# Kernel optimization log

Measured on AMD Instinct MI355X. Metric: run time of the kernel, lower is better.

Reference implementation:

```python
import jax, jax.numpy as jnp
import numpy as np

N = 65536          # query points (rays * samples per chunk)
C = 2048           # num_codes in code cloud
K = 16             # knn neighbors
CD = 64            # code_dim
IN_XYZ = 63        # positional-encoded xyz channels
IN_DIR = 27        # positional-encoded dir channels
W = 128            # decoder width (D=4, skips=[2])
DIST_SCALE = 2.0


def setup_inputs() -> dict:
    key = jax.random.key(0)
    ks = jax.random.split(key, 16)

    def glorot(k, shape):
        return jax.random.normal(k, shape, jnp.float32) / np.float32(np.sqrt(shape[0]))

    in_x = CD + IN_XYZ  # decoder in_channels_xyz = 127
    inp = {
        "indices": jnp.zeros((1,), jnp.int32),
        "query_points": jax.random.uniform(ks[0], (N, 3), jnp.float32),
        "xyzdir_embedded": jax.random.normal(ks[1], (N, IN_XYZ + IN_DIR), jnp.float32),
        "codes_position": jax.random.uniform(ks[2], (1, C, 3), jnp.float32),
        "codes": jax.random.normal(ks[3], (1, C, CD), jnp.float32) * 0.01,
        # decoder params
        "W0": glorot(ks[4], (in_x, W)), "b0": jnp.zeros((W,), jnp.float32),
        "W1": glorot(ks[5], (W, W)), "b1": jnp.zeros((W,), jnp.float32),
        "W2": glorot(ks[6], (W + in_x, W)), "b2": jnp.zeros((W,), jnp.float32),  # skip layer i=2
        "W3": glorot(ks[7], (W, W)), "b3": jnp.zeros((W,), jnp.float32),
        "Wf": glorot(ks[8], (W, W)), "bf": jnp.zeros((W,), jnp.float32),          # xyz_encoding_final
        "Wd": glorot(ks[9], (W + IN_DIR, W // 2)), "bd": jnp.zeros((W // 2,), jnp.float32),
        "Ws": glorot(ks[10], (W, 1)), "bs": jnp.zeros((1,), jnp.float32),
        "Wr": glorot(ks[11], (W // 2, 3)), "br": jnp.zeros((3,), jnp.float32),
    }
    return inp


def _knn_idx(q, c, k):
    # brute-force L2 knn (faiss replacement); indices only, no grad (torch no_grad)
    q = jax.lax.stop_gradient(q)
    c = jax.lax.stop_gradient(c)
    d2 = (jnp.sum(q * q, -1, keepdims=True)
          - 2.0 * q @ c.T
          + jnp.sum(c * c, -1))  # (N, C)
    _, idx = jax.lax.top_k(-d2, k)  # (N, K) nearest
    return idx


def reference(indices, query_points, xyzdir_embedded, codes_position, codes,
              W0, b0, W1, b1, W2, b2, W3, b3, Wf, bf, Wd, bd, Ws, bs, Wr, br):
    # --- CodeCloud.query ---
    cp = codes_position[indices][0]      # (C, 3)
    cc = codes[indices][0]               # (C, CD)
    idx = _knn_idx(query_points, cp, K)  # (N, K)
    neigh_pos = cp[idx]                  # (N, K, 3)
    sq = jnp.sum((query_points[:, None, :] - neigh_pos) ** 2, -1) + 1e-16  # (N, K)
    w = 1.0 / jnp.sqrt(sq) ** DIST_SCALE
    w = w / jnp.sum(w, -1, keepdims=True)
    neigh_codes = cc[idx]                # (N, K, CD)
    query_codes = jnp.einsum("nk,nkd->nd", w, neigh_codes)  # (N, CD)

    # --- IM_Decoder (D=4, W=128, skips=[2]) ---
    x = jnp.concatenate([query_codes, xyzdir_embedded], -1)  # (N, 127+27)
    in_x = CD + IN_XYZ
    input_xyz, input_dir = x[:, :in_x], x[:, in_x:]
    h = jax.nn.relu(input_xyz @ W0 + b0)
    h = jax.nn.relu(h @ W1 + b1)
    h = jax.nn.relu(jnp.concatenate([input_xyz, h], -1) @ W2 + b2)  # skip at i=2
    h = jax.nn.relu(h @ W3 + b3)
    sigma = h @ Ws + bs                       # (N, 1)
    final = h @ Wf + bf                       # (N, W)
    d = jax.nn.relu(jnp.concatenate([final, input_dir], -1) @ Wd + bd)
    rgb = d @ Wr + br                         # (N, 3)
    return jnp.concatenate([rgb, sigma], -1)  # (N, 4)
```

## Files before the change

### kernel.cpp

```cpp
#include <hip/hip_runtime.h>

#define N_Q   65536
#define N_C   2048
#define KNN_K 16
#define CDIM  64
#define SLCAP 128
#define KINF  0x7FFFFFFF

typedef _Float16 half_t;
typedef float v4f __attribute__((ext_vector_type(4)));
typedef half_t v8h __attribute__((ext_vector_type(8)));

#define ASTRIDE 136
#define DSTRIDE 40

__global__ void wtrans_kernel(const float* W0, const float* W1, const float* W2,
                              const float* W3, const float* Wf, const float* Wd,
                              const int* indices, const float* cpos,
                              half_t* wt, float4* cpos4){
  int idx = blockIdx.x * 256 + threadIdx.x;
  if (idx >= 110592) return;
  if (idx >= 108544){
    int i = idx - 108544;
    const float* cp = cpos + (size_t)indices[0] * N_C * 3;
    float x = cp[i*3 + 0], y = cp[i*3 + 1], z = cp[i*3 + 2];
    cpos4[i] = make_float4(x, y, z, fmaf(x, x, fmaf(y, y, fmaf(z, z, 4.0f))));
    return;
  }
  int base, nt, mode;
  const float* src = W1;
  if (idx < 16384){ base = 0; nt = 8; mode = 1; }
  else if (idx < 32768){ base = 16384; nt = 8; mode = 0; src = W1; }
  else if (idx < 65536){ base = 32768; nt = 8; mode = 2; }
  else if (idx < 81920){ base = 65536; nt = 8; mode = 0; src = W3; }
  else if (idx < 98304){ base = 81920; nt = 8; mode = 0; src = Wf; }
  else { base = 98304; nt = 4; mode = 3; }
  int i = idx - base;
  int tile = i >> 9, e = i & 511;
  int lane = e >> 3, j = e & 7;
  int k0idx = tile / nt, tcol = tile - k0idx*nt;
  int n = tcol*16 + (lane & 15);
  int k = k0idx*32 + ((lane >> 4) << 3) + j;
  float val;
  if (mode == 0)      val = src[k*128 + n];
  else if (mode == 1) val = (k < 127) ? W0[k*128 + n] : 0.f;
  else if (mode == 2) val = (k == 127) ? 0.f
                           : ((k < 127) ? W2[k*128 + n] : W2[(k-1)*128 + n]);
  else                val = (k < 155) ? Wd[k*64 + n] : 0.f;
  wt[idx] = (half_t)val;
}

__global__ __launch_bounds__(512, 8) void knn_kernel(const int* indices,
    const float* qpts, const float4* cpos4, const float* codes,
    const float* xyzdir, half_t* Ain, half_t* Din){
  __shared__ float4 lp[N_C];
  __shared__ int    sl[8*SLCAP];
  int tid = threadIdx.x;
  int lane = tid & 63, wave = tid >> 6;
  int l = lane & 15;
  const float* cc = codes + (size_t)indices[0] * N_C * CDIM;

  for (int c = tid; c < N_C; c += 512) lp[c] = cpos4[c];
  __syncthreads();

  int q = blockIdx.x * 8 + wave;
  float qx = qpts[q*3 + 0];
  float qy = qpts[q*3 + 1];
  float qz = qpts[q*3 + 2];
  float nqx = -2.0f*qx, nqy = -2.0f*qy, nqz = -2.0f*qz;

  int p[32];
#pragma unroll
  for (int j = 0; j < 32; j++){
    int c = j*64 + lane;
    float4 P = lp[c];
    float s = fmaf(P.x, nqx, fmaf(P.y, nqy, fmaf(P.z, nqz, P.w)));
    p[j] = (__float_as_int(s) & 0xFFFFF800) | c;
  }

  int lm = p[0];
#pragma unroll
  for (int j = 1; j < 32; j++) lm = min(lm, p[j]);

  int v = lm;
#pragma unroll
  for (int k = 2; k <= 16; k <<= 1){
#pragma unroll
    for (int j = k >> 1; j > 0; j >>= 1){
      int o = __shfl_xor(v, j, 64);
      bool dirDesc = (l & k) != 0;
      bool lower   = (l & j) == 0;
      int mn = min(v, o), mx = max(v, o);
      v = (lower != dirDesc) ? mn : mx;
    }
  }
  int t0 = __shfl(v, 3, 64),  t1 = __shfl(v, 19, 64);
  int t2 = __shfl(v, 35, 64), t3 = __shfl(v, 51, 64);
  int tau = max(max(t0, t1), max(t2, t3));

  int* slw = &sl[wave * SLCAP];
  int n = 0;
#pragma unroll
  for (int j = 0; j < 32; j++){
    bool c = (p[j] <= tau);
    unsigned long long m = __ballot(c);
    if (m){
      if (n <= 64){
        if (c){
          int mb = __builtin_amdgcn_mbcnt_hi((unsigned)(m >> 32),
                   __builtin_amdgcn_mbcnt_lo((unsigned)m, 0));
          slw[n + mb] = p[j];
        }
      }
      n += (int)__popcll(m);
    }
  }
  __builtin_amdgcn_wave_barrier();

  int keep;
  if (n >= KNN_K && n <= 64){
    int x = (lane < n) ? slw[lane] : KINF;
#pragma unroll
    for (int k = 2; k <= 16; k <<= 1){
#pragma unroll
      for (int j = k >> 1; j > 0; j >>= 1){
        int o = __shfl_xor(x, j, 64);
        bool dirDesc = (l & k) != 0;
        bool lower   = (l & j) == 0;
        int mn = min(x, o), mx = max(x, o);
        x = (lower != dirDesc) ? mn : mx;
      }
    }
    x = min(x, __shfl_xor(x, 31, 64));
#pragma unroll
    for (int j = 8; j > 0; j >>= 1){
      int o = __shfl_xor(x, j, 64);
      bool lower = (l & j) == 0;
      int mn = min(x, o), mx = max(x, o);
      x = lower ? mn : mx;
    }
    x = min(x, __shfl_xor(x, 63, 64));
    keep = x;
  } else {
    keep = KINF;
#pragma unroll 1
    for (int rr = 0; rr < KNN_K; rr++){
      int lmf = p[0];
#pragma unroll
      for (int j = 1; j < 32; j++) lmf = min(lmf, p[j]);
      int gm = lmf;
#pragma unroll
      for (int off2 = 1; off2 < 64; off2 <<= 1)
        gm = min(gm, __shfl_xor(gm, off2, 64));
      if (lane == rr) keep = gm;
#pragma unroll
      for (int j = 0; j < 32; j++) p[j] = (p[j] == gm) ? KINF : p[j];
    }
  }

  int ci = keep & 0x7FF;
  float4 P = lp[ci];
  float dx = qx - P.x, dy = qy - P.y, dz = qz - P.z;
  float d2 = fmaf(dz, dz, fmaf(dy, dy, dx*dx));
  float w = 1.0f / (d2 + 1e-16f);
  float wm = (lane < KNN_K) ? w : 0.0f;
#pragma unroll
  for (int off2 = 1; off2 < 64; off2 <<= 1) wm += __shfl_xor(wm, off2, 64);
  float wn = w / wm;

  float acc = 0.f;
#pragma unroll
  for (int i = 0; i < KNN_K; i++){
    int   cb = __shfl(ci, i, 64);
    float wb = __shfl(wn, i, 64);
    acc = fmaf(wb, cc[cb*CDIM + lane], acc);
  }
  size_t arow = (size_t)q * ASTRIDE;
  Ain[arow + lane] = (half_t)acc;

  float xv = (lane < 63) ? xyzdir[(size_t)q*90 + lane] : 0.f;
  Ain[arow + 64 + lane] = (half_t)xv;
  if (lane < 8) Ain[arow + 128 + lane] = (half_t)0.f;
  if (lane < 40){
    float dv = (lane < 27) ? xyzdir[(size_t)q*90 + 63 + lane] : 0.f;
    Din[(size_t)q*DSTRIDE + lane] = (half_t)dv;
  }
}

template<int NT>
__device__ inline void mfma_sw(const half_t* act, int astride, int rowbase,
                               const half_t* wlayer, int nt, int ktbase,
                               int tcolbase, int kchunk, v4f* acc, int lane){
  int m = lane & 15, quad = lane >> 4;
#pragma unroll
  for (int k0 = 0; k0 < kchunk; k0 += 32){
    v8h a = *(const v8h*)&act[(rowbase + m)*astride + k0 + quad*8];
    int krow = ktbase + (k0 >> 5);
#pragma unroll
    for (int t = 0; t < NT; t++){
      const half_t* bp = wlayer + ((size_t)((krow*nt + tcolbase + t) << 9) + (lane << 3));
      v8h b = *(const v8h*)bp;
      acc[t] = __builtin_amdgcn_mfma_f32_16x16x32_f16(a, b, acc[t], 0, 0, 0);
    }
  }
}

template<int NT>
__device__ inline void epilogue(v4f* acc, half_t* outb, int rowbase, int colbase,
                                const float* bias, bool relu, int lane){
  int n = lane & 15, quad = lane >> 4;
#pragma unroll
  for (int t = 0; t < NT; t++){
    int col = colbase + t*16 + n;
    float bv = bias[col];
#pragma unroll
    for (int r = 0; r < 4; r++){
      float v = acc[t][r] + bv;
      if (relu) v = fmaxf(v, 0.f);
      outb[(rowbase + quad*4 + r)*ASTRIDE + col] = (half_t)v;
    }
  }
}

__global__ __launch_bounds__(256) void mlp_mfma(
    const half_t* Ain, const half_t* Din, const half_t* wt,
    const float* b0, const float* b1, const float* b2, const float* b3,
    const float* bfb, const float* bdb,
    const float* Wsb, const float* bsb, const float* Wrb, const float* brb,
    float* out){
  __shared__ __align__(16) half_t Abuf[32*ASTRIDE];
  __shared__ __align__(16) half_t Pbuf[32*ASTRIDE];
  __shared__ __align__(16) half_t Qbuf[32*ASTRIDE];
  __shared__ __align__(16) half_t Dbuf[32*DSTRIDE];

  int tid = threadIdx.x, lane = tid & 63, wave = tid >> 6;
  int qbase = blockIdx.x * 32;

  for (int i = tid; i < 32*17; i += 256){
    int r = i / 17, c8 = i - r*17;
    *(uint4*)&Abuf[r*ASTRIDE + (c8 << 3)] =
        *(const uint4*)&Ain[(size_t)(qbase + r)*ASTRIDE + (c8 << 3)];
  }
  for (int i = tid; i < 32*5; i += 256){
    int r = i / 5, c8 = i - r*5;
    *(uint4*)&Dbuf[r*DSTRIDE + (c8 << 3)] =
        *(const uint4*)&Din[(size_t)(qbase + r)*DSTRIDE + (c8 << 3)];
  }
  __syncthreads();

  int rowbase = (wave >> 1) * 16;
  int colhalf = wave & 1;
  int colbase = colhalf * 64;
  int tcolbase = colhalf * 4;
  v4f acc[4];

  const half_t* wt0 = wt;
  const half_t* wt1 = wt + 16384;
  const half_t* wt2 = wt + 32768;
  const half_t* wt3 = wt + 65536;
  const half_t* wtf = wt + 81920;
  const half_t* wtd = wt + 98304;

#define ZACC4() { for (int t_ = 0; t_ < 4; t_++) for (int e_ = 0; e_ < 4; e_++) acc[t_][e_] = 0.f; }

  ZACC4();
  mfma_sw<4>(Abuf, ASTRIDE, rowbase, wt0, 8, 0, tcolbase, 128, acc, lane);
  epilogue<4>(acc, Pbuf, rowbase, colbase, b0, true, lane);
  __syncthreads();

  ZACC4();
  mfma_sw<4>(Pbuf, ASTRIDE, rowbase, wt1, 8, 0, tcolbase, 128, acc, lane);
  epilogue<4>(acc, Qbuf, rowbase, colbase, b1, true, lane);
  __syncthreads();

  ZACC4();
  mfma_sw<4>(Abuf, ASTRIDE, rowbase, wt2, 8, 0, tcolbase, 128, acc, lane);
  mfma_sw<4>(Qbuf, ASTRIDE, rowbase, wt2, 8, 4, tcolbase, 128, acc, lane);
  epilogue<4>(acc, Pbuf, rowbase, colbase, b2, true, lane);
  __syncthreads();

  ZACC4();
  mfma_sw<4>(Pbuf, ASTRIDE, rowbase, wt3, 8, 0, tcolbase, 128, acc, lane);
  epilogue<4>(acc, Abuf, rowbase, colbase, b3, true, lane);
  __syncthreads();

  ZACC4();
  mfma_sw<4>(Abuf, ASTRIDE, rowbase, wtf, 8, 0, tcolbase, 128, acc, lane);
  epilogue<4>(acc, Pbuf, rowbase, colbase, bfb, false, lane);
  __syncthreads();

  int tcolbase_d = colhalf * 2;
  int colbase_d  = colhalf * 32;
  ZACC4();
  mfma_sw<2>(Pbuf, ASTRIDE, rowbase, wtd, 4, 0, tcolbase_d, 128, acc, lane);
  mfma_sw<2>(Dbuf, DSTRIDE, rowbase, wtd, 4, 4, tcolbase_d,  32, acc, lane);
  epilogue<2>(acc, Qbuf, rowbase, colbase_d, bdb, true, lane);
  __syncthreads();

  {
    int q = tid >> 3, part = tid & 7;
    float s = 0.f;
#pragma unroll
    for (int k = 0; k < 16; k++){
      int kk = part*16 + k;
      s = fmaf((float)Abuf[q*ASTRIDE + kk], Wsb[kk], s);
    }
    s += __shfl_xor(s, 1, 64); s += __shfl_xor(s, 2, 64); s += __shfl_xor(s, 4, 64);

    float r3[3];
#pragma unroll
    for (int c2 = 0; c2 < 3; c2++){
      float rv = 0.f;
#pragma unroll
      for (int k = 0; k < 8; k++){
        int kk = part*8 + k;
        rv = fmaf((float)Qbuf[q*ASTRIDE + kk], Wrb[kk*3 + c2], rv);
      }
      rv += __shfl_xor(rv, 1, 64); rv += __shfl_xor(rv, 2, 64); rv += __shfl_xor(rv, 4, 64);
      r3[c2] = rv;
    }
    if (part == 0){
      size_t ob = ((size_t)(qbase + q)) * 4;
      out[ob + 0] = r3[0] + brb[0];
      out[ob + 1] = r3[1] + brb[1];
      out[ob + 2] = r3[2] + brb[2];
      out[ob + 3] = s + bsb[0];
    }
  }
}

extern "C" void kernel_launch(void* const* d_in, const int* in_sizes, int n_in,
                              void* d_out, int out_size, void* d_ws, size_t ws_size,
                              hipStream_t stream){
  (void)in_sizes; (void)n_in; (void)out_size; (void)ws_size;

  const int*   indices = (const int*)d_in[0];
  const float* qpts    = (const float*)d_in[1];
  const float* xyzdir  = (const float*)d_in[2];
  const float* cpos    = (const float*)d_in[3];
  const float* codes   = (const float*)d_in[4];
  const float* W0 = (const float*)d_in[5];
  const float* b0 = (const float*)d_in[6];
  const float* W1 = (const float*)d_in[7];
  const float* b1 = (const float*)d_in[8];
  const float* W2 = (const float*)d_in[9];
  const float* b2 = (const float*)d_in[10];
  const float* W3 = (const float*)d_in[11];
  const float* b3 = (const float*)d_in[12];
  const float* Wf = (const float*)d_in[13];
  const float* bf = (const float*)d_in[14];
  const float* Wd = (const float*)d_in[15];
  const float* bd = (const float*)d_in[16];
  const float* Ws = (const float*)d_in[17];
  const float* bs = (const float*)d_in[18];
  const float* Wr = (const float*)d_in[19];
  const float* br = (const float*)d_in[20];

  half_t* Ain   = (half_t*)d_ws;
  half_t* Din   = (half_t*)((char*)d_ws + 17825792);
  half_t* wt    = (half_t*)((char*)d_ws + 17825792 + 5242880);
  float4* cpos4 = (float4*)((char*)d_ws + 17825792 + 5242880 + 217088);

  wtrans_kernel<<<(110592 + 255)/256, 256, 0, stream>>>(W0, W1, W2, W3, Wf, Wd,
                                                        indices, cpos, wt, cpos4);
  knn_kernel<<<N_Q/8, 512, 0, stream>>>(indices, qpts, cpos4, codes, xyzdir,
                                        Ain, Din);
  mlp_mfma<<<N_Q/32, 256, 0, stream>>>(Ain, Din, wt,
                                       b0, b1, b2, b3, bf, bd, Ws, bs, Wr, br,
                                       (float*)d_out);
}
```

Baseline: 232.0 us.

## Process two queries per wave in KNN and replicate MLP weights

The KNN kernel now has each wave handle two queries. Every code-position LDS read is reused for two distance computations, and the grid is halved, with launch bounds relaxed to 4 blocks. Separately, the transposed fp16 weights are written in four copies, and MLP blocks pick a copy by block index to spread global/L2 traffic on the shared weights. The cost is higher register pressure from two 32-entry candidate arrays, possible lower occupancy, and extra workspace.

New measurement: 678.6 us. +192.5%, slower.

```diff
diff --git a/kernel.cpp b/kernel.cpp
--- a/kernel.cpp
+++ b/kernel.cpp
@@ -6,6 +6,8 @@
 #define CDIM  64
 #define SLCAP 128
 #define KINF  0x7FFFFFFF
+#define WREP  4
+#define WSZ   108544
 
 typedef _Float16 half_t;
 typedef float v4f __attribute__((ext_vector_type(4)));
@@ -20,8 +22,8 @@
                               half_t* wt, float4* cpos4){
   int idx = blockIdx.x * 256 + threadIdx.x;
   if (idx >= 110592) return;
-  if (idx >= 108544){
-    int i = idx - 108544;
+  if (idx >= WSZ){
+    int i = idx - WSZ;
     const float* cp = cpos + (size_t)indices[0] * N_C * 3;
     float x = cp[i*3 + 0], y = cp[i*3 + 1], z = cp[i*3 + 2];
     cpos4[i] = make_float4(x, y, z, fmaf(x, x, fmaf(y, y, fmaf(z, z, 4.0f))));
@@ -47,37 +49,12 @@
   else if (mode == 2) val = (k == 127) ? 0.f
                            : ((k < 127) ? W2[k*128 + n] : W2[(k-1)*128 + n]);
   else                val = (k < 155) ? Wd[k*64 + n] : 0.f;
-  wt[idx] = (half_t)val;
-}
-
-__global__ __launch_bounds__(512, 8) void knn_kernel(const int* indices,
-    const float* qpts, const float4* cpos4, const float* codes,
-    const float* xyzdir, half_t* Ain, half_t* Din){
-  __shared__ float4 lp[N_C];
-  __shared__ int    sl[8*SLCAP];
-  int tid = threadIdx.x;
-  int lane = tid & 63, wave = tid >> 6;
-  int l = lane & 15;
-  const float* cc = codes + (size_t)indices[0] * N_C * CDIM;
-
-  for (int c = tid; c < N_C; c += 512) lp[c] = cpos4[c];
-  __syncthreads();
-
-  int q = blockIdx.x * 8 + wave;
-  float qx = qpts[q*3 + 0];
-  float qy = qpts[q*3 + 1];
-  float qz = qpts[q*3 + 2];
-  float nqx = -2.0f*qx, nqy = -2.0f*qy, nqz = -2.0f*qz;
-
-  int p[32];
-#pragma unroll
-  for (int j = 0; j < 32; j++){
-    int c = j*64 + lane;
-    float4 P = lp[c];
-    float s = fmaf(P.x, nqx, fmaf(P.y, nqy, fmaf(P.z, nqz, P.w)));
-    p[j] = (__float_as_int(s) & 0xFFFFF800) | c;
-  }
-
+  half_t hv = (half_t)val;
+#pragma unroll
+  for (int rp = 0; rp < WREP; rp++) wt[rp*WSZ + idx] = hv;
+}
+
+__device__ inline int select16(int* p, int* slw, int lane, int l){
   int lm = p[0];
 #pragma unroll
   for (int j = 1; j < 32; j++) lm = min(lm, p[j]);
@@ -98,7 +75,6 @@
   int t2 = __shfl(v, 35, 64), t3 = __shfl(v, 51, 64);
   int tau = max(max(t0, t1), max(t2, t3));
 
-  int* slw = &sl[wave * SLCAP];
   int n = 0;
 #pragma unroll
   for (int j = 0; j < 32; j++){
@@ -157,33 +133,78 @@
       for (int j = 0; j < 32; j++) p[j] = (p[j] == gm) ? KINF : p[j];
     }
   }
-
-  int ci = keep & 0x7FF;
-  float4 P = lp[ci];
-  float dx = qx - P.x, dy = qy - P.y, dz = qz - P.z;
-  float d2 = fmaf(dz, dz, fmaf(dy, dy, dx*dx));
-  float w = 1.0f / (d2 + 1e-16f);
-  float wm = (lane < KNN_K) ? w : 0.0f;
-#pragma unroll
-  for (int off2 = 1; off2 < 64; off2 <<= 1) wm += __shfl_xor(wm, off2, 64);
-  float wn = w / wm;
-
-  float acc = 0.f;
-#pragma unroll
-  for (int i = 0; i < KNN_K; i++){
-    int   cb = __shfl(ci, i, 64);
-    float wb = __shfl(wn, i, 64);
-    acc = fmaf(wb, cc[cb*CDIM + lane], acc);
-  }
-  size_t arow = (size_t)q * ASTRIDE;
-  Ain[arow + lane] = (half_t)acc;
-
-  float xv = (lane < 63) ? xyzdir[(size_t)q*90 + lane] : 0.f;
-  Ain[arow + 64 + lane] = (half_t)xv;
-  if (lane < 8) Ain[arow + 128 + lane] = (half_t)0.f;
-  if (lane < 40){
-    float dv = (lane < 27) ? xyzdir[(size_t)q*90 + 63 + lane] : 0.f;
-    Din[(size_t)q*DSTRIDE + lane] = (half_t)dv;
+  return keep;
+}
+
+__global__ __launch_bounds__(512, 4) void knn_kernel(const int* indices,
+    const float* qpts, const float4* cpos4, const float* codes,
+    const float* xyzdir, half_t* Ain, half_t* Din){
+  __shared__ float4 lp[N_C];
+  __shared__ int    sl[16*SLCAP];
+  int tid = threadIdx.x;
+  int lane = tid & 63, wave = tid >> 6;
+  int l = lane & 15;
+  const float* cc = codes + (size_t)indices[0] * N_C * CDIM;
+
+  for (int c = tid; c < N_C; c += 512) lp[c] = cpos4[c];
+  __syncthreads();
+
+  int q0 = blockIdx.x * 16 + wave * 2;
+  int q1 = q0 + 1;
+  float qx0 = qpts[q0*3+0], qy0 = qpts[q0*3+1], qz0 = qpts[q0*3+2];
+  float qx1 = qpts[q1*3+0], qy1 = qpts[q1*3+1], qz1 = qpts[q1*3+2];
+  float nx0 = -2.f*qx0, ny0 = -2.f*qy0, nz0 = -2.f*qz0;
+  float nx1 = -2.f*qx1, ny1 = -2.f*qy1, nz1 = -2.f*qz1;
+
+  int p0[32], p1[32];
+#pragma unroll
+  for (int j = 0; j < 32; j++){
+    int c = j*64 + lane;
+    float4 P = lp[c];
+    float s0 = fmaf(P.x, nx0, fmaf(P.y, ny0, fmaf(P.z, nz0, P.w)));
+    float s1 = fmaf(P.x, nx1, fmaf(P.y, ny1, fmaf(P.z, nz1, P.w)));
+    p0[j] = (__float_as_int(s0) & 0xFFFFF800) | c;
+    p1[j] = (__float_as_int(s1) & 0xFFFFF800) | c;
+  }
+
+  int keep0 = select16(p0, &sl[(wave*2 + 0) * SLCAP], lane, l);
+  int keep1 = select16(p1, &sl[(wave*2 + 1) * SLCAP], lane, l);
+
+#pragma unroll
+  for (int qq = 0; qq < 2; qq++){
+    int q = (qq == 0) ? q0 : q1;
+    int keep = (qq == 0) ? keep0 : keep1;
+    float qx = (qq == 0) ? qx0 : qx1;
+    float qy = (qq == 0) ? qy0 : qy1;
+    float qz = (qq == 0) ? qz0 : qz1;
+
+    int ci = keep & 0x7FF;
+    float4 P = lp[ci];
+    float dx = qx - P.x, dy = qy - P.y, dz = qz - P.z;
+    float d2 = fmaf(dz, dz, fmaf(dy, dy, dx*dx));
+    float w = 1.0f / (d2 + 1e-16f);
+    float wm = (lane < KNN_K) ? w : 0.0f;
+#pragma unroll
+    for (int off2 = 1; off2 < 64; off2 <<= 1) wm += __shfl_xor(wm, off2, 64);
+    float wn = w / wm;
+
+    float acc = 0.f;
+#pragma unroll
+    for (int i = 0; i < KNN_K; i++){
+      int   cb = __shfl(ci, i, 64);
+      float wb = __shfl(wn, i, 64);
+      acc = fmaf(wb, cc[cb*CDIM + lane], acc);
+    }
+    size_t arow = (size_t)q * ASTRIDE;
+    Ain[arow + lane] = (half_t)acc;
+
+    float xv = (lane < 63) ? xyzdir[(size_t)q*90 + lane] : 0.f;
+    Ain[arow + 64 + lane] = (half_t)xv;
+    if (lane < 8) Ain[arow + 128 + lane] = (half_t)0.f;
+    if (lane < 40){
+      float dv = (lane < 27) ? xyzdir[(size_t)q*90 + 63 + lane] : 0.f;
+      Din[(size_t)q*DSTRIDE + lane] = (half_t)dv;
+    }
   }
 }
 
@@ -223,7 +244,7 @@
 }
 
 __global__ __launch_bounds__(256) void mlp_mfma(
-    const half_t* Ain, const half_t* Din, const half_t* wt,
+    const half_t* Ain, const half_t* Din, const half_t* wtg,
     const float* b0, const float* b1, const float* b2, const float* b3,
     const float* bfb, const float* bdb,
     const float* Wsb, const float* bsb, const float* Wrb, const float* brb,
@@ -235,6 +256,7 @@
 
   int tid = threadIdx.x, lane = tid & 63, wave = tid >> 6;
   int qbase = blockIdx.x * 32;
+  const half_t* wt = wtg + (size_t)((blockIdx.x >> 3) & (WREP - 1)) * WSZ;
 
   for (int i = tid; i < 32*17; i += 256){
     int r = i / 17, c8 = i - r*17;
@@ -359,12 +381,12 @@
   half_t* Ain   = (half_t*)d_ws;
   half_t* Din   = (half_t*)((char*)d_ws + 17825792);
   half_t* wt    = (half_t*)((char*)d_ws + 17825792 + 5242880);
-  float4* cpos4 = (float4*)((char*)d_ws + 17825792 + 5242880 + 217088);
+  float4* cpos4 = (float4*)((char*)d_ws + 17825792 + 5242880 + (size_t)WREP*WSZ*2);
 
   wtrans_kernel<<<(110592 + 255)/256, 256, 0, stream>>>(W0, W1, W2, W3, Wf, Wd,
                                                         indices, cpos, wt, cpos4);
-  knn_kernel<<<N_Q/8, 512, 0, stream>>>(indices, qpts, cpos4, codes, xyzdir,
-                                        Ain, Din);
+  knn_kernel<<<N_Q/16, 512, 0, stream>>>(indices, qpts, cpos4, codes, xyzdir,
+                                         Ain, Din);
   mlp_mfma<<<N_Q/32, 256, 0, stream>>>(Ain, Din, wt,
                                        b0, b1, b2, b3, bf, bd, Ws, bs, Wr, br,
                                        (float*)d_out);
```
